# Optimization experiments

Measured on AMD Instinct MI355X. Metric: run time of the kernel, lower is better.

The kernel has to match this reference:

```python
import jax, jax.numpy as jnp
import numpy as np

CH = 128
GROUPS = 8
EPS = 1e-5

def group_norm(x, w, b):
    B, C, H, W = x.shape
    g = x.reshape(B, GROUPS, C // GROUPS, H, W)
    mean = g.mean(axis=(2, 3, 4), keepdims=True)
    var = g.var(axis=(2, 3, 4), keepdims=True)
    g = (g - mean) * jax.lax.rsqrt(var + EPS)
    g = g.reshape(B, C, H, W)
    return g * w[None, :, None, None] + b[None, :, None, None]

def setup_inputs() -> dict:
    key = jax.random.key(0)
    ks = jax.random.split(key, 7)
    C = CH
    x = jax.random.normal(ks[0], (8, C, 64, 64), dtype=jnp.float32)
    gn_w = jnp.ones((C,), dtype=jnp.float32)
    gn_b = jnp.zeros((C,), dtype=jnp.float32)
    s = 1.0 / np.sqrt(C)
    qkv_w = jax.random.normal(ks[1], (3 * C, C), dtype=jnp.float32) * s
    qkv_b = jax.random.normal(ks[2], (3 * C,), dtype=jnp.float32) * 0.01
    proj_w = jax.random.normal(ks[3], (C, C), dtype=jnp.float32) * s
    proj_b = jax.random.normal(ks[4], (C,), dtype=jnp.float32) * 0.01
    return {"x": x, "gn_w": gn_w, "gn_b": gn_b, "qkv_w": qkv_w,
            "qkv_b": qkv_b, "proj_w": proj_w, "proj_b": proj_b}

def reference(x, gn_w, gn_b, qkv_w, qkv_b, proj_w, proj_b):
    B, C, H, W = x.shape
    h = group_norm(x, gn_w, gn_b)
    # 1x1 conv == per-pixel matmul over channels
    qkv = jnp.einsum('bchw,oc->bohw', h, qkv_w) + qkv_b[None, :, None, None]
    q, k, v = jnp.split(qkv.reshape(B, 3 * C, H * W), 3, axis=1)  # each [B,C,N]
    scale = C ** (-0.5)
    attn = jax.nn.softmax(jnp.einsum('bci,bcj->bij', q * scale, k), axis=-1)
    out = jnp.einsum('bij,bcj->bci', attn, v).reshape(B, C, H, W)
    out = jnp.einsum('bchw,oc->bohw', out, proj_w) + proj_b[None, :, None, None]
    return x + out
```

## Files before the change

### kernel.cpp

```cpp
#include <hip/hip_runtime.h>
#include <stdint.h>


typedef __attribute__((ext_vector_type(8))) short short8;
typedef __attribute__((ext_vector_type(4))) float f32x4;
typedef __attribute__((ext_vector_type(16))) float f32x16;

#define MFMA_BF16(a, b, c) __builtin_amdgcn_mfma_f32_16x16x32_bf16((a), (b), (c), 0, 0, 0)
#define MFMA32(a, b, c) __builtin_amdgcn_mfma_f32_32x32x16_bf16((a), (b), (c), 0, 0, 0)
#define EXP2(x) __builtin_amdgcn_exp2f(x)

#define QSCALE 0.12751743f

__device__ __forceinline__ unsigned short f2bf(float f) {
    unsigned int u = __builtin_bit_cast(unsigned int, f);
    u += 0x7FFFu + ((u >> 16) & 1u);
    return (unsigned short)(u >> 16);
}
__device__ __forceinline__ float bf2f(unsigned int lo16) {
    return __builtin_bit_cast(float, lo16 << 16);
}
__device__ __forceinline__ short8 ldg8(const unsigned short* p) {
    return __builtin_bit_cast(short8, *(const uint4*)p);
}
__device__ __forceinline__ unsigned int cvtpk(float lo, float hi) {
    unsigned int r;
    asm("v_cvt_pk_bf16_f32 %0, %1, %2" : "=v"(r) : "v"(lo), "v"(hi));
    return r;
}
__device__ __forceinline__ void gload16(const void* g, void* l) {
    __builtin_amdgcn_global_load_lds(
        (__attribute__((address_space(1))) void*)g,
        (__attribute__((address_space(3))) void*)l, 16, 0, 0);
}

__global__ __launch_bounds__(256) void k_pre(const float* __restrict__ x,
                                             float* __restrict__ sums,
                                             const float* __restrict__ qkv_w,
                                             const float* __restrict__ proj_w,
                                             unsigned short* __restrict__ wq,
                                             unsigned short* __restrict__ wp) {
    if (blockIdx.x >= 1024) {
        int i = ((blockIdx.x - 1024) * 256 + threadIdx.x) * 4;
        const float* src; unsigned short* dst; int off;
        if (i < 49152) { src = qkv_w; dst = wq; off = i; }
        else           { src = proj_w; dst = wp; off = i - 49152; }
        float4 v = *(const float4*)(src + off);
        uint2 pk;
        pk.x = (unsigned int)f2bf(v.x) | ((unsigned int)f2bf(v.y) << 16);
        pk.y = (unsigned int)f2bf(v.z) | ((unsigned int)f2bf(v.w) << 16);
        *(uint2*)(dst + off) = pk;
        return;
    }
    int g     = blockIdx.x >> 4;
    int slice = blockIdx.x & 15;
    const float* p = x + (size_t)g * 65536 + slice * 4096;
    float s = 0.f, sq = 0.f;
#pragma unroll
    for (int i = 0; i < 4; ++i) {
        float4 v = *(const float4*)(p + threadIdx.x * 4 + i * 1024);
        s  += v.x + v.y + v.z + v.w;
        sq += v.x*v.x + v.y*v.y + v.z*v.z + v.w*v.w;
    }
#pragma unroll
    for (int m = 1; m < 64; m <<= 1) { s += __shfl_xor(s, m, 64); sq += __shfl_xor(sq, m, 64); }
    __shared__ float ss[4], ssq[4];
    int w = threadIdx.x >> 6;
    if ((threadIdx.x & 63) == 0) { ss[w] = s; ssq[w] = sq; }
    __syncthreads();
    if (threadIdx.x == 0) {
        atomicAdd(&sums[g * 2],     ss[0] + ss[1] + ss[2] + ss[3]);
        atomicAdd(&sums[g * 2 + 1], ssq[0] + ssq[1] + ssq[2] + ssq[3]);
    }
}

__global__ __launch_bounds__(256) void k_qkv(const float* __restrict__ x,
                                             const float* __restrict__ sums,
                                             const float* __restrict__ gn_w,
                                             const float* __restrict__ gn_b,
                                             const unsigned short* __restrict__ wq,
                                             const float* __restrict__ qkv_b,
                                             unsigned short* __restrict__ q_ws,
                                             unsigned short* __restrict__ k_ws,
                                             unsigned short* __restrict__ v_ws) {
    __shared__ unsigned short h_lds[64][136];
    const int tid  = threadIdx.x;
    const int b    = blockIdx.x >> 6;
    const int n0   = (blockIdx.x & 63) << 6;
    const int lane = tid & 63, wave = tid >> 6;
    const int l15  = lane & 15, q4 = lane >> 4;

    {
        int cb = tid >> 4;
        int nn = (tid & 15) << 2;
#pragma unroll
        for (int k = 0; k < 8; ++k) {
            int c = cb + (k << 4);
            float4 v = *(const float4*)(x + ((size_t)(b * 128 + c) << 12) + n0 + nn);
            int g = c >> 4;
            float ts = sums[(b * 8 + g) * 2];
            float tq = sums[(b * 8 + g) * 2 + 1];
            float mean = ts * (1.f / 65536.f);
            float var  = tq * (1.f / 65536.f) - mean * mean;
            float rstd = rsqrtf(var + 1e-5f);
            float ga = gn_w[c] * rstd;
            float be = gn_b[c] - mean * ga;
            h_lds[nn + 0][c] = f2bf(v.x * ga + be);
            h_lds[nn + 1][c] = f2bf(v.y * ga + be);
            h_lds[nn + 2][c] = f2bf(v.z * ga + be);
            h_lds[nn + 3][c] = f2bf(v.w * ga + be);
        }
    }
    __syncthreads();

    short8 bfrag[4][4];
#pragma unroll
    for (int nt = 0; nt < 4; ++nt)
#pragma unroll
        for (int ks = 0; ks < 4; ++ks)
            bfrag[nt][ks] = *(const short8*)&h_lds[nt * 16 + l15][ks * 32 + q4 * 8];

#pragma unroll
    for (int ot = 0; ot < 6; ++ot) {
        int o0 = wave * 96 + ot * 16;
        short8 af[4];
#pragma unroll
        for (int ks = 0; ks < 4; ++ks)
            af[ks] = ldg8(wq + (size_t)(o0 + l15) * 128 + ks * 32 + q4 * 8);

        if (o0 < 256) {
            float bias[4];
#pragma unroll
            for (int r = 0; r < 4; ++r) bias[r] = qkv_b[o0 + q4 * 4 + r];
            float qs = (o0 < 128) ? QSCALE : 1.0f;
#pragma unroll
            for (int nt = 0; nt < 4; ++nt) {
                f32x4 acc = {0.f, 0.f, 0.f, 0.f};
#pragma unroll
                for (int ks = 0; ks < 4; ++ks)
                    acc = MFMA_BF16(af[ks], bfrag[nt][ks], acc);
                int n = n0 + nt * 16 + l15;
                unsigned short* dst = (o0 < 128) ? q_ws : k_ws;
                int oo = (o0 < 128) ? o0 : (o0 - 128);
                unsigned int lo = (unsigned int)f2bf((acc[0] + bias[0]) * qs) |
                                  ((unsigned int)f2bf((acc[1] + bias[1]) * qs) << 16);
                unsigned int hi = (unsigned int)f2bf((acc[2] + bias[2]) * qs) |
                                  ((unsigned int)f2bf((acc[3] + bias[3]) * qs) << 16);
                uint2 pk; pk.x = lo; pk.y = hi;
                *(uint2*)&dst[((size_t)(b * 4096 + n) << 7) + oo + q4 * 4] = pk;
            }
        } else {
            int c = o0 - 256 + l15;
            float vb = qkv_b[o0 + l15];
            unsigned short* vrow = v_ws + ((size_t)(b * 128 + c) << 12) + n0;
#pragma unroll
            for (int nt = 0; nt < 4; ++nt) {
                f32x4 acc = {0.f, 0.f, 0.f, 0.f};
#pragma unroll
                for (int ks = 0; ks < 4; ++ks)
                    acc = MFMA_BF16(bfrag[nt][ks], af[ks], acc);
                unsigned int lo = (unsigned int)f2bf(acc[0] + vb) |
                                  ((unsigned int)f2bf(acc[1] + vb) << 16);
                unsigned int hi = (unsigned int)f2bf(acc[2] + vb) |
                                  ((unsigned int)f2bf(acc[3] + vb) << 16);
                uint2 pk; pk.x = lo; pk.y = hi;
                *(uint2*)&vrow[nt * 16 + q4 * 4] = pk;
            }
        }
    }
}

__global__ __launch_bounds__(256, 2) void k_attn_part(const unsigned short* __restrict__ q_ws,
                                                      const unsigned short* __restrict__ k_ws,
                                                      const unsigned short* __restrict__ v_ws,
                                                      unsigned short* __restrict__ o_part,
                                                      float* __restrict__ ml) {
    __shared__ unsigned short K0[64][128];
    __shared__ unsigned short K1[64][128];
    __shared__ unsigned short V0[128][64];
    __shared__ unsigned short V1[128][64];
    __shared__ unsigned short P_lds[64][72];
    __shared__ float Lp[128];

    const int tid   = threadIdx.x;
    const int chunk = blockIdx.x & 3;
    const int tile  = (blockIdx.x >> 2) & 63;
    const int b     = blockIdx.x >> 8;
    const int i0    = tile << 6;
    const int lane  = tid & 63, wave = tid >> 6;
    const int ih    = wave >> 1, jh = wave & 1;
    const int l31   = lane & 31, h = lane >> 5;

    short8 qf[8];
    {
        const unsigned short* qp =
            q_ws + ((size_t)(b * 4096 + i0 + ih * 32 + l31) << 7) + h * 8;
#pragma unroll
        for (int ks = 0; ks < 8; ++ks) qf[ks] = ldg8(qp + ks * 16);
    }

    f32x16 acc[2];
#pragma unroll
    for (int e = 0; e < 16; ++e) { acc[0][e] = 0.f; acc[1][e] = 0.f; }
    float l_run = 0.f;

    const unsigned short* kbase = k_ws + ((size_t)b << 19) + ((size_t)chunk << 17);
    int ksrcChunk[4];
#pragma unroll
    for (int q = 0; q < 4; ++q) {
        int c   = wave * 256 + q * 64 + lane;
        int row = c >> 4;
        ksrcChunk[q] = row * 16 + ((c & 15) ^ (row & 15));
    }
    const unsigned short* vbase = v_ws + ((size_t)b << 19) +
        ((size_t)(wave * 32 + (lane >> 3)) << 12) +
        ((((lane & 7) ^ (lane >> 3))) << 3) + (chunk << 10);

#define STAGE(T, KD, VD)                                                              \
  do {                                                                                \
    _Pragma("unroll")                                                                 \
    for (int q = 0; q < 4; ++q)                                                       \
      gload16(kbase + (size_t)(T) * 8192 + ksrcChunk[q] * 8,                          \
              (char*)(&KD[0][0]) + wave * 4096 + q * 1024);                           \
    _Pragma("unroll")                                                                 \
    for (int q = 0; q < 4; ++q)                                                       \
      gload16(vbase + (size_t)q * 32768 + (T) * 64,                                   \
              (char*)(&VD[0][0]) + (wave * 4 + q) * 1024);                            \
  } while (0)

    const int krow = jh * 32 + l31;
    const int ksw  = krow & 15;
    const int vsw  = l31 & 7;

    STAGE(0, K0, V0);

#define ATTN_ITER(IT, KR, VR, KP, VP)                                                 \
  do {                                                                                \
    __syncthreads(); \
    if ((IT) < 15) STAGE((IT) + 1, KP, VP);      \
    f32x16 s;           \
    _Pragma("unroll")                                                                 \
    for (int e = 0; e < 16; ++e) s[e] = 0.f;                                          \
    _Pragma("unroll")                                                                 \
    for (int ks = 0; ks < 8; ++ks) {                                                  \
      short8 kf = *(const short8*)&KR[krow][((ks * 2 + h) ^ ksw) << 3];               \
      s = MFMA32(kf, qf[ks], s);                                                      \
    }                                                                                 \
    float pv[16];                                        \
    _Pragma("unroll")                                                                 \
    for (int e = 0; e < 16; ++e) pv[e] = EXP2(fminf(s[e], 30.f));                     \
    l_run += (((pv[0] + pv[1]) + (pv[2] + pv[3])) +                                   \
              ((pv[4] + pv[5]) + (pv[6] + pv[7]))) +                                  \
             (((pv[8] + pv[9]) + (pv[10] + pv[11])) +                                 \
              ((pv[12] + pv[13]) + (pv[14] + pv[15])));                               \
    {                                                                                 \
      unsigned short* prow = &P_lds[ih * 32 + l31][jh * 32 + (h << 2)];               \
      _Pragma("unroll")                                                               \
      for (int rr = 0; rr < 4; ++rr) {                                                \
        uint2 pk;                                                                     \
        pk.x = cvtpk(pv[rr * 4 + 0], pv[rr * 4 + 1]);                                 \
        pk.y = cvtpk(pv[rr * 4 + 2], pv[rr * 4 + 3]);                                 \
        *(uint2*)(prow + rr * 8) = pk;                                                \
      }                                                                               \
    }                                                                                 \
    __syncthreads();      \
    _Pragma("unroll")                                                                 \
    for (int ks = 0; ks < 4; ++ks) {                                                  \
      short8 pf = *(const short8*)&P_lds[ih * 32 + l31][ks * 16 + h * 8];             \
      _Pragma("unroll")                                                               \
      for (int ct = 0; ct < 2; ++ct) {                                                \
        short8 vf = *(const short8*)                                                  \
            &VR[jh * 64 + ct * 32 + l31][((ks * 2 + h) ^ vsw) << 3];                  \
        acc[ct] = MFMA32(pf, vf, acc[ct]);                                            \
      }                                                                               \
    }                                                                                 \
  } while (0)

    for (int ib = 0; ib < 8; ++ib) {
        ATTN_ITER(ib * 2,     K0, V0, K1, V1);
        ATTN_ITER(ib * 2 + 1, K1, V1, K0, V0);
    }
#undef ATTN_ITER
#undef STAGE

    float l2 = l_run + __shfl_xor(l_run, 32);
    if (h == 0) Lp[jh * 64 + ih * 32 + l31] = l2;
    __syncthreads();

    size_t pbase = (size_t)((b * 64 + tile) * 4 + chunk) * 8192;
    float rl[16];
#pragma unroll
    for (int r = 0; r < 16; ++r) {
        int il = (r & 3) + ((r >> 2) << 3) + (h << 2);
        rl[r] = 1.0f / (Lp[ih * 32 + il] + Lp[64 + ih * 32 + il]);
    }
#pragma unroll
    for (int ct = 0; ct < 2; ++ct)
#pragma unroll
        for (int r = 0; r < 16; ++r) {
            int row = ih * 32 + (r & 3) + ((r >> 2) << 3) + (h << 2);
            o_part[pbase + (size_t)row * 128 + jh * 64 + ct * 32 + l31] =
                f2bf(acc[ct][r] * rl[r]);
        }
    if (tid < 64) {
        int mb = ((b * 64 + tile) * 4 + chunk) * 64;
        ml[mb + tid] = __log2f(Lp[tid] + Lp[64 + tid]);
    }
}

__global__ __launch_bounds__(256) void k_merge_proj(const unsigned short* __restrict__ o_part,
                                                    const float* __restrict__ ml,
                                                    const float* __restrict__ x,
                                                    const unsigned short* __restrict__ wp,
                                                    const float* __restrict__ proj_b,
                                                    float* __restrict__ out) {
    __shared__ unsigned short O_lds[64][136];
    __shared__ float wgt[64][4];
    const int tid  = threadIdx.x;
    const int b    = blockIdx.x >> 6;
    const int tile = blockIdx.x & 63;
    const int i0   = tile << 6;
    const int lane = tid & 63, wave = tid >> 6;
    const int l15  = lane & 15, q4 = lane >> 4;
    const int tb   = (b * 64 + tile) * 4;

    if (tid < 64) {
        float m0 = ml[(tb + 0) * 64 + tid], m1 = ml[(tb + 1) * 64 + tid];
        float m2 = ml[(tb + 2) * 64 + tid], m3 = ml[(tb + 3) * 64 + tid];
        float M = fmaxf(fmaxf(m0, m1), fmaxf(m2, m3));
        float w0 = EXP2(m0 - M), w1 = EXP2(m1 - M), w2 = EXP2(m2 - M), w3 = EXP2(m3 - M);
        float rW = 1.0f / (w0 + w1 + w2 + w3);
        wgt[tid][0] = w0 * rW; wgt[tid][1] = w1 * rW;
        wgt[tid][2] = w2 * rW; wgt[tid][3] = w3 * rW;
    }
    __syncthreads();

    {
        int n = tid >> 2, q = tid & 3;
        float w[4];
#pragma unroll
        for (int ch = 0; ch < 4; ++ch) w[ch] = wgt[n][ch];
#pragma unroll
        for (int g = 0; g < 4; ++g) {
            float acc[8];
#pragma unroll
            for (int e = 0; e < 8; ++e) acc[e] = 0.f;
#pragma unroll
            for (int ch = 0; ch < 4; ++ch) {
                const unsigned short* p =
                    o_part + (size_t)(tb + ch) * 8192 + (size_t)n * 128 + q * 32 + g * 8;
                uint4 v = *(const uint4*)p;
                float wc = w[ch];
                acc[0] += wc * bf2f(v.x & 0xFFFF); acc[1] += wc * bf2f(v.x >> 16);
                acc[2] += wc * bf2f(v.y & 0xFFFF); acc[3] += wc * bf2f(v.y >> 16);
                acc[4] += wc * bf2f(v.z & 0xFFFF); acc[5] += wc * bf2f(v.z >> 16);
                acc[6] += wc * bf2f(v.w & 0xFFFF); acc[7] += wc * bf2f(v.w >> 16);
            }
            uint4 pk;
            pk.x = (unsigned int)f2bf(acc[0]) | ((unsigned int)f2bf(acc[1]) << 16);
            pk.y = (unsigned int)f2bf(acc[2]) | ((unsigned int)f2bf(acc[3]) << 16);
            pk.z = (unsigned int)f2bf(acc[4]) | ((unsigned int)f2bf(acc[5]) << 16);
            pk.w = (unsigned int)f2bf(acc[6]) | ((unsigned int)f2bf(acc[7]) << 16);
            *(uint4*)&O_lds[n][q * 32 + g * 8] = pk;
        }
    }
    __syncthreads();

    short8 bfrag[4][4];
#pragma unroll
    for (int nt = 0; nt < 4; ++nt)
#pragma unroll
        for (int ks = 0; ks < 4; ++ks)
            bfrag[nt][ks] = *(const short8*)&O_lds[nt * 16 + l15][ks * 32 + q4 * 8];

#pragma unroll
    for (int ot = 0; ot < 2; ++ot) {
        int o0 = wave * 32 + ot * 16;
        short8 af[4];
#pragma unroll
        for (int ks = 0; ks < 4; ++ks)
            af[ks] = ldg8(wp + (size_t)(o0 + l15) * 128 + ks * 32 + q4 * 8);
        float pb[4];
#pragma unroll
        for (int r = 0; r < 4; ++r) pb[r] = proj_b[o0 + q4 * 4 + r];

#pragma unroll
        for (int nt = 0; nt < 4; ++nt) {
            f32x4 acc = {0.f, 0.f, 0.f, 0.f};
#pragma unroll
            for (int ks = 0; ks < 4; ++ks)
                acc = MFMA_BF16(af[ks], bfrag[nt][ks], acc);
#pragma unroll
            for (int r = 0; r < 4; ++r) {
                size_t idx = ((size_t)(b * 128 + o0 + q4 * 4 + r) << 12) + i0 + nt * 16 + l15;
                out[idx] = x[idx] + acc[r] + pb[r];
            }
        }
    }
}

extern "C" void kernel_launch(void* const* d_in, const int* in_sizes, int n_in,
                              void* d_out, int out_size, void* d_ws, size_t ws_size,
                              hipStream_t stream) {
    const float* x      = (const float*)d_in[0];
    const float* gn_w   = (const float*)d_in[1];
    const float* gn_b   = (const float*)d_in[2];
    const float* qkv_w  = (const float*)d_in[3];
    const float* qkv_b  = (const float*)d_in[4];
    const float* proj_w = (const float*)d_in[5];
    const float* proj_b = (const float*)d_in[6];
    float* out = (float*)d_out;

    char* ws = (char*)d_ws;
    float* sums           = (float*)ws;
    unsigned short* wq    = (unsigned short*)(ws + 4096);
    unsigned short* wp    = (unsigned short*)(ws + 4096 + 98304);
    unsigned short* q_ws  = (unsigned short*)(ws + ((size_t)1  << 20));
    unsigned short* k_ws  = (unsigned short*)(ws + ((size_t)9  << 20));
    unsigned short* v_ws  = (unsigned short*)(ws + ((size_t)17 << 20));
    unsigned short* o_part= (unsigned short*)(ws + ((size_t)25 << 20));
    float* ml             = (float*)(ws + ((size_t)57 << 20));

    hipMemsetAsync(sums, 0, 512, stream);
    k_pre<<<1088, 256, 0, stream>>>(x, sums, qkv_w, proj_w, wq, wp);
    k_qkv<<<512, 256, 0, stream>>>(x, sums, gn_w, gn_b, wq, qkv_b, q_ws, k_ws, v_ws);
    k_attn_part<<<2048, 256, 0, stream>>>(q_ws, k_ws, v_ws, o_part, ml);
    k_merge_proj<<<512, 256, 0, stream>>>(o_part, ml, x, wp, proj_b, out);
}
```

Baseline: 208.3 us.

## Enlarge attention query tile to 128 rows with 512-thread blocks sharing K/V tiles

```diff
diff --git a/kernel.cpp b/kernel.cpp
--- a/kernel.cpp
+++ b/kernel.cpp
@@ -170,7 +170,7 @@
     }
 }
 
-__global__ __launch_bounds__(256, 2) void k_attn_part(const unsigned short* __restrict__ q_ws,
+__global__ __launch_bounds__(512, 4) void k_attn_part(const unsigned short* __restrict__ q_ws,
                                                       const unsigned short* __restrict__ k_ws,
                                                       const unsigned short* __restrict__ v_ws,
                                                       unsigned short* __restrict__ o_part,
@@ -179,14 +179,13 @@
     __shared__ unsigned short K1[64][128];
     __shared__ unsigned short V0[128][64];
     __shared__ unsigned short V1[128][64];
-    __shared__ unsigned short P_lds[64][72];
-    __shared__ float Lp[128];
+    __shared__ unsigned short P_lds[128][64];
 
     const int tid   = threadIdx.x;
     const int chunk = blockIdx.x & 3;
-    const int tile  = (blockIdx.x >> 2) & 63;
-    const int b     = blockIdx.x >> 8;
-    const int i0    = tile << 6;
+    const int tile  = (blockIdx.x >> 2) & 31;
+    const int b     = blockIdx.x >> 7;
+    const int i0    = tile << 7;
     const int lane  = tid & 63, wave = tid >> 6;
     const int ih    = wave >> 1, jh = wave & 1;
     const int l31   = lane & 31, h = lane >> 5;
@@ -205,40 +204,42 @@
     float l_run = 0.f;
 
     const unsigned short* kbase = k_ws + ((size_t)b << 19) + ((size_t)chunk << 17);
-    int ksrcChunk[4];
-#pragma unroll
-    for (int q = 0; q < 4; ++q) {
-        int c   = wave * 256 + q * 64 + lane;
+    int ksrc[2];
+#pragma unroll
+    for (int q = 0; q < 2; ++q) {
+        int c   = q * 512 + tid;
         int row = c >> 4;
-        ksrcChunk[q] = row * 16 + ((c & 15) ^ (row & 15));
-    }
-    const unsigned short* vbase = v_ws + ((size_t)b << 19) +
-        ((size_t)(wave * 32 + (lane >> 3)) << 12) +
-        ((((lane & 7) ^ (lane >> 3))) << 3) + (chunk << 10);
+        ksrc[q] = row * 16 + ((c & 15) ^ (row & 15));
+    }
+    const unsigned short* vlane = v_ws + ((size_t)b << 19) +
+        ((size_t)(tid >> 3) << 12) + (chunk << 10) +
+        ((((tid & 7) ^ ((tid >> 3) & 7) ^ wave)) << 3);
 
 #define STAGE(T, KD, VD)                                                              \
   do {                                                                                \
     _Pragma("unroll")                                                                 \
-    for (int q = 0; q < 4; ++q)                                                       \
-      gload16(kbase + (size_t)(T) * 8192 + ksrcChunk[q] * 8,                          \
-              (char*)(&KD[0][0]) + wave * 4096 + q * 1024);                           \
-    _Pragma("unroll")                                                                 \
-    for (int q = 0; q < 4; ++q)                                                       \
-      gload16(vbase + (size_t)q * 32768 + (T) * 64,                                   \
-              (char*)(&VD[0][0]) + (wave * 4 + q) * 1024);                            \
+    for (int q = 0; q < 2; ++q)                                                       \
+      gload16(kbase + (size_t)(T) * 8192 + ksrc[q] * 8,                               \
+              (char*)(&KD[0][0]) + q * 8192 + wave * 1024);                           \
+    _Pragma("unroll")                                                                 \
+    for (int q = 0; q < 2; ++q)                                                       \
+      gload16(vlane + (size_t)q * 262144 + (T) * 64,                                  \
+              (char*)(&VD[0][0]) + q * 8192 + wave * 1024);                           \
   } while (0)
 
     const int krow = jh * 32 + l31;
-    const int ksw  = krow & 15;
-    const int vsw  = l31 & 7;
+    const int ksw  = l31 & 15;
+    const int vk   = (l31 & 7) ^ (l31 >> 3);
+    const int irow = ih * 32 + l31;
+    const int pkey = (irow ^ (irow >> 3)) & 7;
 
     STAGE(0, K0, V0);
 
 #define ATTN_ITER(IT, KR, VR, KP, VP)                                                 \
   do {                                                                                \
-    __syncthreads(); \
-    if ((IT) < 15) STAGE((IT) + 1, KP, VP);      \
-    f32x16 s;           \
+    __syncthreads();        \
+    if ((IT) < 15) STAGE((IT) + 1, KP, VP);     \
+    f32x16 s;        \
     _Pragma("unroll")                                                                 \
     for (int e = 0; e < 16; ++e) s[e] = 0.f;                                          \
     _Pragma("unroll")                                                                 \
@@ -254,23 +255,24 @@
              (((pv[8] + pv[9]) + (pv[10] + pv[11])) +                                 \
               ((pv[12] + pv[13]) + (pv[14] + pv[15])));                               \
     {                                                                                 \
-      unsigned short* prow = &P_lds[ih * 32 + l31][jh * 32 + (h << 2)];               \
+      char* prow = (char*)&P_lds[irow][0];                                            \
       _Pragma("unroll")                                                               \
       for (int rr = 0; rr < 4; ++rr) {                                                \
         uint2 pk;                                                                     \
         pk.x = cvtpk(pv[rr * 4 + 0], pv[rr * 4 + 1]);                                 \
         pk.y = cvtpk(pv[rr * 4 + 2], pv[rr * 4 + 3]);                                 \
-        *(uint2*)(prow + rr * 8) = pk;                                                \
+        *(uint2*)(prow + ((((jh << 2) + rr) ^ pkey) << 4) + (h << 3)) = pk;           \
       }                                                                               \
     }                                                                                 \
-    __syncthreads();      \
+    __syncthreads();                                                \
     _Pragma("unroll")                                                                 \
     for (int ks = 0; ks < 4; ++ks) {                                                  \
-      short8 pf = *(const short8*)&P_lds[ih * 32 + l31][ks * 16 + h * 8];             \
+      short8 pf = *(const short8*)((const char*)&P_lds[irow][0] +                     \
+                                   (((ks * 2 + h) ^ pkey) << 4));                     \
       _Pragma("unroll")                                                               \
       for (int ct = 0; ct < 2; ++ct) {                                                \
-        short8 vf = *(const short8*)                                                  \
-            &VR[jh * 64 + ct * 32 + l31][((ks * 2 + h) ^ vsw) << 3];                  \
+        short8 vf = *(const short8*)&VR[jh * 64 + ct * 32 + l31]                      \
+                        [((ks * 2 + h) ^ vk ^ (ct << 2)) << 3];                       \
         acc[ct] = MFMA32(pf, vf, acc[ct]);                                            \
       }                                                                               \
     }                                                                                 \
@@ -283,28 +285,28 @@
 #undef ATTN_ITER
 #undef STAGE
 
+    __syncthreads();
+    float* Lp = (float*)(&K0[0][0]);
     float l2 = l_run + __shfl_xor(l_run, 32);
-    if (h == 0) Lp[jh * 64 + ih * 32 + l31] = l2;
-    __syncthreads();
-
-    size_t pbase = (size_t)((b * 64 + tile) * 4 + chunk) * 8192;
+    if (h == 0) Lp[jh * 128 + irow] = l2;
+    __syncthreads();
+
     float rl[16];
 #pragma unroll
     for (int r = 0; r < 16; ++r) {
         int il = (r & 3) + ((r >> 2) << 3) + (h << 2);
-        rl[r] = 1.0f / (Lp[ih * 32 + il] + Lp[64 + ih * 32 + il]);
+        rl[r] = 1.0f / (Lp[ih * 32 + il] + Lp[128 + ih * 32 + il]);
     }
 #pragma unroll
     for (int ct = 0; ct < 2; ++ct)
 #pragma unroll
         for (int r = 0; r < 16; ++r) {
             int row = ih * 32 + (r & 3) + ((r >> 2) << 3) + (h << 2);
-            o_part[pbase + (size_t)row * 128 + jh * 64 + ct * 32 + l31] =
-                f2bf(acc[ct][r] * rl[r]);
+            o_part[(((size_t)(b * 4096 + i0 + row) * 4 + chunk) << 7) +
+                   jh * 64 + ct * 32 + l31] = f2bf(acc[ct][r] * rl[r]);
         }
-    if (tid < 64) {
-        int mb = ((b * 64 + tile) * 4 + chunk) * 64;
-        ml[mb + tid] = __log2f(Lp[tid] + Lp[64 + tid]);
+    if (tid < 128) {
+        ml[(b * 4096 + i0 + tid) * 4 + chunk] = __log2f(Lp[tid] + Lp[128 + tid]);
     }
 }
 
@@ -322,11 +324,10 @@
     const int i0   = tile << 6;
     const int lane = tid & 63, wave = tid >> 6;
     const int l15  = lane & 15, q4 = lane >> 4;
-    const int tb   = (b * 64 + tile) * 4;
 
     if (tid < 64) {
-        float m0 = ml[(tb + 0) * 64 + tid], m1 = ml[(tb + 1) * 64 + tid];
-        float m2 = ml[(tb + 2) * 64 + tid], m3 = ml[(tb + 3) * 64 + tid];
+        size_t mb = (size_t)(b * 4096 + i0 + tid) * 4;
+        float m0 = ml[mb + 0], m1 = ml[mb + 1], m2 = ml[mb + 2], m3 = ml[mb + 3];
         float M = fmaxf(fmaxf(m0, m1), fmaxf(m2, m3));
         float w0 = EXP2(m0 - M), w1 = EXP2(m1 - M), w2 = EXP2(m2 - M), w3 = EXP2(m3 - M);
         float rW = 1.0f / (w0 + w1 + w2 + w3);
@@ -340,6 +341,7 @@
         float w[4];
 #pragma unroll
         for (int ch = 0; ch < 4; ++ch) w[ch] = wgt[n][ch];
+        size_t rbase = ((size_t)(b * 4096 + i0 + n) * 4) << 7;
 #pragma unroll
         for (int g = 0; g < 4; ++g) {
             float acc[8];
@@ -347,8 +349,7 @@
             for (int e = 0; e < 8; ++e) acc[e] = 0.f;
 #pragma unroll
             for (int ch = 0; ch < 4; ++ch) {
-                const unsigned short* p =
-                    o_part + (size_t)(tb + ch) * 8192 + (size_t)n * 128 + q * 32 + g * 8;
+                const unsigned short* p = o_part + rbase + (ch << 7) + q * 32 + g * 8;
                 uint4 v = *(const uint4*)p;
                 float wc = w[ch];
                 acc[0] += wc * bf2f(v.x & 0xFFFF); acc[1] += wc * bf2f(v.x >> 16);
@@ -424,6 +425,6 @@
     hipMemsetAsync(sums, 0, 512, stream);
     k_pre<<<1088, 256, 0, stream>>>(x, sums, qkv_w, proj_w, wq, wp);
     k_qkv<<<512, 256, 0, stream>>>(x, sums, gn_w, gn_b, wq, qkv_b, q_ws, k_ws, v_ws);
-    k_attn_part<<<2048, 256, 0, stream>>>(q_ws, k_ws, v_ws, o_part, ml);
+    k_attn_part<<<1024, 512, 0, stream>>>(q_ws, k_ws, v_ws, o_part, ml);
     k_merge_proj<<<512, 256, 0, stream>>>(o_part, ml, x, wp, proj_b, out);
 }
```

After: 230.7 us. +10.8%, slower.
